# Optimization experiments

Measured on AMD Instinct MI355X. Metric: run time of the kernel, lower is better.

Reference implementation:

```python
import jax, jax.numpy as jnp
import numpy as np

N, E = 50000, 800000
F_IN, HID, H, LBL = 512, 16, 8, 40
HC = HID * H  # 128
BN_EPS = 1e-5
ELU_ALPHA = 0.2
NEG_SLOPE = 0.2


def setup_inputs() -> dict:
    key = jax.random.key(0)
    ks = jax.random.split(key, 32)
    inp = {}
    inp['x'] = jax.random.normal(ks[0], (N, F_IN), dtype=jnp.float32)
    inp['edge_index'] = jax.random.randint(ks[1], (2, E), 0, N, dtype=jnp.int32)
    # layer 0: F_IN -> (H, HID), concat
    inp['W0'] = jax.random.normal(ks[2], (F_IN, HC), dtype=jnp.float32) * 0.05
    inp['as0'] = jax.random.normal(ks[3], (H, HID), dtype=jnp.float32) * 0.1
    inp['ad0'] = jax.random.normal(ks[4], (H, HID), dtype=jnp.float32) * 0.1
    inp['b0'] = jnp.zeros((HC,), jnp.float32)
    inp['g0'] = jnp.ones((HC,), jnp.float32)
    inp['be0'] = jnp.zeros((HC,), jnp.float32)
    inp['rm0'] = jnp.zeros((HC,), jnp.float32)
    inp['rv0'] = jnp.ones((HC,), jnp.float32)
    # layer 1: HC -> (H, HID), concat
    inp['W1'] = jax.random.normal(ks[5], (HC, HC), dtype=jnp.float32) * 0.1
    inp['as1'] = jax.random.normal(ks[6], (H, HID), dtype=jnp.float32) * 0.1
    inp['ad1'] = jax.random.normal(ks[7], (H, HID), dtype=jnp.float32) * 0.1
    inp['b1'] = jnp.zeros((HC,), jnp.float32)
    inp['g1'] = jnp.ones((HC,), jnp.float32)
    inp['be1'] = jnp.zeros((HC,), jnp.float32)
    inp['rm1'] = jnp.zeros((HC,), jnp.float32)
    inp['rv1'] = jnp.ones((HC,), jnp.float32)
    # layer 2: HC -> (1, LBL), mean (concat=False)
    inp['W2'] = jax.random.normal(ks[8], (HC, LBL), dtype=jnp.float32) * 0.1
    inp['as2'] = jax.random.normal(ks[9], (1, LBL), dtype=jnp.float32) * 0.1
    inp['ad2'] = jax.random.normal(ks[10], (1, LBL), dtype=jnp.float32) * 0.1
    inp['b2'] = jnp.zeros((LBL,), jnp.float32)
    return inp


def _gat_conv(xf, src, dst, W, a_src, a_dst, b, heads, out_ch, concat):
    # PyG GATConv (eval): linear -> per-head attn logits -> segment softmax over dst -> scatter-add
    n = xf.shape[0]
    h = (xf @ W).reshape(n, heads, out_ch)            # [N,H,C]
    alpha_s = jnp.einsum('nhc,hc->nh', h, a_src)      # [N,H]
    alpha_d = jnp.einsum('nhc,hc->nh', h, a_dst)
    e = jax.nn.leaky_relu(alpha_s[src] + alpha_d[dst], NEG_SLOPE)  # [Etot,H]
    m = jax.ops.segment_max(e, dst, num_segments=n)
    e = jnp.exp(e - m[dst])
    s = jax.ops.segment_sum(e, dst, num_segments=n)
    alpha = e / (s[dst] + 1e-16)                      # [Etot,H]
    msg = alpha[:, :, None] * h[src]                  # [Etot,H,C]
    out = jax.ops.segment_sum(msg, dst, num_segments=n)  # [N,H,C]
    out = out.reshape(n, heads * out_ch) if concat else out.mean(axis=1)
    return out + b


def _bn_elu(xf, g, be, rm, rv):
    y = (xf - rm) * (g * jax.lax.rsqrt(rv + BN_EPS)) + be
    return jnp.where(y > 0, y, ELU_ALPHA * jnp.expm1(y))


def reference(x, edge_index, W0, as0, ad0, b0, g0, be0, rm0, rv0,
              W1, as1, ad1, b1, g1, be1, rm1, rv1, W2, as2, ad2, b2):
    n = x.shape[0]
    # add self-loops (PyG GATConv default add_self_loops=True)
    loops = jnp.arange(n, dtype=edge_index.dtype)
    src = jnp.concatenate([edge_index[0], loops])
    dst = jnp.concatenate([edge_index[1], loops])
    h = _gat_conv(x, src, dst, W0, as0, ad0, b0, H, HID, True)
    h = _bn_elu(h, g0, be0, rm0, rv0)
    h = _gat_conv(h, src, dst, W1, as1, ad1, b1, H, HID, True)
    h = _bn_elu(h, g1, be1, rm1, rv1)
    out = _gat_conv(h, src, dst, W2, as2, ad2, b2, 1, LBL, False)
    return out
```

## Files before the change

kernel.cpp:

```cpp
#include <hip/hip_runtime.h>
#include <hip/hip_bf16.h>
#include <cstdint>
#include <cstddef>

#define NN 50000
#define EE 800000
#define FIN 512
#define HIDC 16
#define NH 8
#define HCH 128
#define NLBL 40
#define NLBLP 48
#define ETOT (EE + NN)
#define NEG_SLOPE 0.2f
#define ELU_A 0.2f
#define BN_EPS 1e-5f

typedef __attribute__((ext_vector_type(8))) short bf16x8;
typedef __attribute__((ext_vector_type(4))) float f32x4;

__device__ inline short f2b(float f) {
    __hip_bfloat16 h = __float2bfloat16(f);
    return *reinterpret_cast<short*>(&h);
}
__device__ inline float blo(unsigned int u) {
    union { unsigned int u; float f; } v; v.u = u << 16; return v.f;
}
__device__ inline float bhi(unsigned int u) {
    union { unsigned int u; float f; } v; v.u = u & 0xffff0000u; return v.f;
}

__global__ __launch_bounds__(256) void k_convW(const float* __restrict__ W,
                                               short* __restrict__ Wt,
                                               int K, int N, int Np)
{
    int idx = blockIdx.x * blockDim.x + threadIdx.x;
    if (idx >= Np * K) return;
    int n = idx / K, k = idx - n * K;
    float v = (n < N) ? W[(size_t)k * N + n] : 0.f;
    Wt[idx] = f2b(v);
}

template<int KDIM, int NTILES, bool A_BF16>
__global__ __launch_bounds__(256) void k_gemm_lds(const void* __restrict__ Ap,
                                                  const short* __restrict__ Wt,
                                                  short* __restrict__ C,
                                                  int M, int N)
{
    constexpr int NFULL = NTILES * 16;
    constexpr int KCH = 128;
    constexpr int NK = KDIM / 32;
    constexpr int NCH = KDIM / KCH;
    constexpr int LROW = KCH + 8;
    __shared__ short Bs[NFULL * LROW];

    const int tid  = threadIdx.x;
    const int wave = tid >> 6;
    const int lane = tid & 63;
    const int quad = lane >> 4;
    const int col  = lane & 15;
    const int cb   = blockIdx.y * NFULL;
    const int row  = blockIdx.x * 64 + wave * 16 + col;
    const int arow = row < M ? row : M - 1;

    f32x4 acc[NTILES];
    #pragma unroll
    for (int t = 0; t < NTILES; ++t) acc[t] = (f32x4){0.f, 0.f, 0.f, 0.f};

    bf16x8 arB[4];
    float4 arF[4][2];
    const short* Ab = (const short*)Ap;
    const float* Af = (const float*)Ap;
    auto pf = [&](int ks) {
        if (ks >= NK) return;
        if (A_BF16) {
            arB[ks & 3] = *(const bf16x8*)(Ab + (size_t)arow * KDIM + ks * 32 + quad * 8);
        } else {
            const float4* p = (const float4*)(Af + (size_t)arow * KDIM + ks * 32 + quad * 8);
            arF[ks & 3][0] = p[0];
            arF[ks & 3][1] = p[1];
        }
    };
    pf(0); pf(1); pf(2); pf(3);

    for (int c = 0; c < NCH; ++c) {
        const int k0 = c * KCH;
        constexpr int TOT8 = NFULL * (KCH / 8);
        #pragma unroll
        for (int i = tid; i < TOT8; i += 256) {
            int n  = i >> 4;
            int kk = i & 15;
            bf16x8 v = *(const bf16x8*)(Wt + (size_t)(cb + n) * KDIM + k0 + kk * 8);
            *(bf16x8*)(Bs + n * LROW + kk * 8) = v;
        }
        __syncthreads();
        #pragma unroll
        for (int s = 0; s < KCH / 32; ++s) {
            const int ks = c * (KCH / 32) + s;
            bf16x8 afrag;
            if (A_BF16) {
                afrag = arB[ks & 3];
            } else {
                float4 v0 = arF[ks & 3][0], v1 = arF[ks & 3][1];
                afrag[0] = f2b(v0.x); afrag[1] = f2b(v0.y);
                afrag[2] = f2b(v0.z); afrag[3] = f2b(v0.w);
                afrag[4] = f2b(v1.x); afrag[5] = f2b(v1.y);
                afrag[6] = f2b(v1.z); afrag[7] = f2b(v1.w);
            }
            pf(ks + 4);
            #pragma unroll
            for (int t = 0; t < NTILES; ++t) {
                bf16x8 bfrag = *(const bf16x8*)(Bs + (t * 16 + col) * LROW + s * 32 + quad * 8);
                acc[t] = __builtin_amdgcn_mfma_f32_16x16x32_bf16(afrag, bfrag, acc[t], 0, 0, 0);
            }
        }
        if (c + 1 < NCH) __syncthreads();
    }

    const int mbase = blockIdx.x * 64 + wave * 16 + quad * 4;
    #pragma unroll
    for (int t = 0; t < NTILES; ++t) {
        int cc = cb + t * 16 + col;
        if (cc < N) {
            #pragma unroll
            for (int r = 0; r < 4; ++r) {
                int m = mbase + r;
                if (m < M) C[(size_t)m * N + cc] = f2b(acc[t][r]);
            }
        }
    }
}

__global__ __launch_bounds__(256) void k_alpha(const unsigned short* __restrict__ h,
                                               const float* __restrict__ a_s,
                                               const float* __restrict__ a_d,
                                               float* __restrict__ as_o,
                                               float* __restrict__ ad_o)
{
    int idx = blockIdx.x * blockDim.x + threadIdx.x;
    if (idx >= NN * NH) return;
    int hh = idx & (NH - 1);
    const uint4* hp = (const uint4*)(h + (size_t)idx * HIDC);
    uint4 q0 = hp[0], q1 = hp[1];
    unsigned int u[8] = {q0.x, q0.y, q0.z, q0.w, q1.x, q1.y, q1.z, q1.w};
    const float* ap = a_s + hh * HIDC;
    const float* dp = a_d + hh * HIDC;
    float ss = 0.f, dd = 0.f;
    #pragma unroll
    for (int i = 0; i < 8; ++i) {
        float f0 = blo(u[i]), f1 = bhi(u[i]);
        ss += f0 * ap[2 * i] + f1 * ap[2 * i + 1];
        dd += f0 * dp[2 * i] + f1 * dp[2 * i + 1];
    }
    as_o[idx] = ss;
    ad_o[idx] = dd;
}

__global__ __launch_bounds__(256) void k_alpha2(const unsigned short* __restrict__ h2,
                                                const float* __restrict__ a_s,
                                                const float* __restrict__ a_d,
                                                float* __restrict__ as_o,
                                                float* __restrict__ ad_o)
{
    int n = blockIdx.x * blockDim.x + threadIdx.x;
    if (n >= NN) return;
    const uint4* hp = (const uint4*)(h2 + (size_t)n * NLBL);
    float ss = 0.f, dd = 0.f;
    #pragma unroll
    for (int qi = 0; qi < 5; ++qi) {
        uint4 q = hp[qi];
        unsigned int u[4] = {q.x, q.y, q.z, q.w};
        #pragma unroll
        for (int j = 0; j < 4; ++j) {
            int c = qi * 8 + j * 2;
            float f0 = blo(u[j]), f1 = bhi(u[j]);
            ss += f0 * a_s[c] + f1 * a_s[c + 1];
            dd += f0 * a_d[c] + f1 * a_d[c + 1];
        }
    }
    as_o[n] = ss;
    ad_o[n] = dd;
}

__global__ __launch_bounds__(256) void k_hist(const int* __restrict__ ei,
                                              int* __restrict__ deg)
{
    int e = blockIdx.x * blockDim.x + threadIdx.x;
    if (e >= ETOT) return;
    int dst = (e < EE) ? ei[EE + e] : (e - EE);
    atomicAdd(&deg[dst], 1);
}

__global__ __launch_bounds__(1024) void k_scan(const int* __restrict__ deg,
                                               int* __restrict__ row_ptr,
                                               int* __restrict__ cursor)
{
    __shared__ int sm[1024];
    __shared__ int carry;
    int tid = threadIdx.x;
    if (tid == 0) carry = 0;
    __syncthreads();
    for (int base = 0; base < NN; base += 8192) {
        int v[8];
        int s = 0;
        int i0 = base + tid * 8;
        #pragma unroll
        for (int j = 0; j < 8; ++j) {
            int i = i0 + j;
            v[j] = (i < NN) ? deg[i] : 0;
            s += v[j];
        }
        sm[tid] = s;
        __syncthreads();
        for (int ofs = 1; ofs < 1024; ofs <<= 1) {
            int t = (tid >= ofs) ? sm[tid - ofs] : 0;
            __syncthreads();
            sm[tid] += t;
            __syncthreads();
        }
        int excl = sm[tid] - s + carry;
        #pragma unroll
        for (int j = 0; j < 8; ++j) {
            int i = i0 + j;
            if (i < NN) { row_ptr[i] = excl; cursor[i] = excl; }
            excl += v[j];
        }
        int total = sm[1023];
        __syncthreads();
        if (tid == 0) carry += total;
        __syncthreads();
    }
    if (tid == 0) row_ptr[NN] = carry;
}

__global__ __launch_bounds__(256) void k_scatter(const int* __restrict__ ei,
                                                 int* __restrict__ cursor,
                                                 int* __restrict__ csr_src)
{
    int e = blockIdx.x * blockDim.x + threadIdx.x;
    if (e >= ETOT) return;
    int src, dst;
    if (e < EE) { src = ei[e]; dst = ei[EE + e]; }
    else        { src = dst = e - EE; }
    int pos = atomicAdd(&cursor[dst], 1);
    csr_src[pos] = src;
}

__global__ __launch_bounds__(256) void k_agg(const int* __restrict__ row_ptr,
                                             const int* __restrict__ csr_src,
                                             const unsigned short* __restrict__ h,
                                             const float* __restrict__ as,
                                             const float* __restrict__ ad,
                                             const float* __restrict__ b,
                                             const float* __restrict__ g,
                                             const float* __restrict__ be,
                                             const float* __restrict__ rm,
                                             const float* __restrict__ rv,
                                             short* __restrict__ out)
{
    int n = blockIdx.x * 4 + (threadIdx.x >> 6);
    if (n >= NN) return;
    int lane = threadIdx.x & 63;
    int half = lane >> 5;
    int c4 = lane & 31;
    int hh = c4 >> 2;
    float adv = ad[n * NH + hh];
    float a0 = 0.f, a1 = 0.f, a2 = 0.f, a3 = 0.f, sw = 0.f;
    int jb = row_ptr[n], je = row_ptr[n + 1];
    int j = jb + half;
    for (; j + 6 < je; j += 8) {
        int s0 = csr_src[j];
        int s1 = csr_src[j + 2];
        int s2 = csr_src[j + 4];
        int s3 = csr_src[j + 6];
        float l0 = as[s0 * NH + hh] + adv;
        float l1 = as[s1 * NH + hh] + adv;
        float l2 = as[s2 * NH + hh] + adv;
        float l3 = as[s3 * NH + hh] + adv;
        uint2 u0 = *(const uint2*)(h + (size_t)s0 * HCH + 4 * c4);
        uint2 u1 = *(const uint2*)(h + (size_t)s1 * HCH + 4 * c4);
        uint2 u2 = *(const uint2*)(h + (size_t)s2 * HCH + 4 * c4);
        uint2 u3 = *(const uint2*)(h + (size_t)s3 * HCH + 4 * c4);
        l0 = l0 > 0.f ? l0 : NEG_SLOPE * l0;
        l1 = l1 > 0.f ? l1 : NEG_SLOPE * l1;
        l2 = l2 > 0.f ? l2 : NEG_SLOPE * l2;
        l3 = l3 > 0.f ? l3 : NEG_SLOPE * l3;
        float w0 = __expf(l0), w1 = __expf(l1), w2 = __expf(l2), w3 = __expf(l3);
        sw += (w0 + w1) + (w2 + w3);
        a0 += w0 * blo(u0.x) + w1 * blo(u1.x) + w2 * blo(u2.x) + w3 * blo(u3.x);
        a1 += w0 * bhi(u0.x) + w1 * bhi(u1.x) + w2 * bhi(u2.x) + w3 * bhi(u3.x);
        a2 += w0 * blo(u0.y) + w1 * blo(u1.y) + w2 * blo(u2.y) + w3 * blo(u3.y);
        a3 += w0 * bhi(u0.y) + w1 * bhi(u1.y) + w2 * bhi(u2.y) + w3 * bhi(u3.y);
    }
    for (; j < je; j += 2) {
        int s0 = csr_src[j];
        float l0 = as[s0 * NH + hh] + adv;
        uint2 u0 = *(const uint2*)(h + (size_t)s0 * HCH + 4 * c4);
        l0 = l0 > 0.f ? l0 : NEG_SLOPE * l0;
        float w0 = __expf(l0);
        sw += w0;
        a0 += w0 * blo(u0.x);
        a1 += w0 * bhi(u0.x);
        a2 += w0 * blo(u0.y);
        a3 += w0 * bhi(u0.y);
    }
    a0 += __shfl_down(a0, 32);
    a1 += __shfl_down(a1, 32);
    a2 += __shfl_down(a2, 32);
    a3 += __shfl_down(a3, 32);
    sw += __shfl_down(sw, 32);
    if (half == 0) {
        int c = 4 * c4;
        float inv = 1.f / (sw + 1e-16f);
        float4 bv  = *(const float4*)(b + c);
        float4 gv  = *(const float4*)(g + c);
        float4 bev = *(const float4*)(be + c);
        float4 rmv = *(const float4*)(rm + c);
        float4 rvv = *(const float4*)(rv + c);
        float r0 = a0 * inv + bv.x;
        float r1 = a1 * inv + bv.y;
        float r2 = a2 * inv + bv.z;
        float r3 = a3 * inv + bv.w;
        r0 = (r0 - rmv.x) * (gv.x * rsqrtf(rvv.x + BN_EPS)) + bev.x;
        r1 = (r1 - rmv.y) * (gv.y * rsqrtf(rvv.y + BN_EPS)) + bev.y;
        r2 = (r2 - rmv.z) * (gv.z * rsqrtf(rvv.z + BN_EPS)) + bev.z;
        r3 = (r3 - rmv.w) * (gv.w * rsqrtf(rvv.w + BN_EPS)) + bev.w;
        r0 = r0 > 0.f ? r0 : ELU_A * expm1f(r0);
        r1 = r1 > 0.f ? r1 : ELU_A * expm1f(r1);
        r2 = r2 > 0.f ? r2 : ELU_A * expm1f(r2);
        r3 = r3 > 0.f ? r3 : ELU_A * expm1f(r3);
        unsigned int lo = (unsigned int)(unsigned short)f2b(r0) |
                          ((unsigned int)(unsigned short)f2b(r1) << 16);
        unsigned int hi = (unsigned int)(unsigned short)f2b(r2) |
                          ((unsigned int)(unsigned short)f2b(r3) << 16);
        *(uint2*)(out + (size_t)n * HCH + c) = make_uint2(lo, hi);
    }
}

__global__ __launch_bounds__(256) void k_agg2(const int* __restrict__ row_ptr,
                                              const int* __restrict__ csr_src,
                                              const unsigned short* __restrict__ h2,
                                              const float* __restrict__ as,
                                              const float* __restrict__ ad,
                                              const float* __restrict__ b,
                                              float* __restrict__ out)
{
    int n = blockIdx.x * 4 + (threadIdx.x >> 6);
    if (n >= NN) return;
    int lane = threadIdx.x & 63;
    int half = lane >> 5;
    int c2 = lane & 31;
    bool act = c2 < 20;
    int coff = act ? 2 * c2 : 0;
    float adv = ad[n];
    float acc0 = 0.f, acc1 = 0.f, sw = 0.f;
    int jb = row_ptr[n], je = row_ptr[n + 1];
    int j = jb + half;
    for (; j + 6 < je; j += 8) {
        int s0 = csr_src[j];
        int s1 = csr_src[j + 2];
        int s2 = csr_src[j + 4];
        int s3 = csr_src[j + 6];
        float l0 = as[s0] + adv;
        float l1 = as[s1] + adv;
        float l2 = as[s2] + adv;
        float l3 = as[s3] + adv;
        unsigned int u0 = *(const unsigned int*)(h2 + (size_t)s0 * NLBL + coff);
        unsigned int u1 = *(const unsigned int*)(h2 + (size_t)s1 * NLBL + coff);
        unsigned int u2 = *(const unsigned int*)(h2 + (size_t)s2 * NLBL + coff);
        unsigned int u3 = *(const unsigned int*)(h2 + (size_t)s3 * NLBL + coff);
        l0 = l0 > 0.f ? l0 : NEG_SLOPE * l0;
        l1 = l1 > 0.f ? l1 : NEG_SLOPE * l1;
        l2 = l2 > 0.f ? l2 : NEG_SLOPE * l2;
        l3 = l3 > 0.f ? l3 : NEG_SLOPE * l3;
        float w0 = __expf(l0), w1 = __expf(l1), w2 = __expf(l2), w3 = __expf(l3);
        sw += (w0 + w1) + (w2 + w3);
        if (act) {
            acc0 += w0 * blo(u0) + w1 * blo(u1) + w2 * blo(u2) + w3 * blo(u3);
            acc1 += w0 * bhi(u0) + w1 * bhi(u1) + w2 * bhi(u2) + w3 * bhi(u3);
        }
    }
    for (; j < je; j += 2) {
        int s = csr_src[j];
        float l = as[s] + adv;
        unsigned int u = *(const unsigned int*)(h2 + (size_t)s * NLBL + coff);
        l = l > 0.f ? l : NEG_SLOPE * l;
        float w = __expf(l);
        sw += w;
        if (act) {
            acc0 += w * blo(u);
            acc1 += w * bhi(u);
        }
    }
    float acc0b = __shfl_down(acc0, 32);
    float acc1b = __shfl_down(acc1, 32);
    float swb   = __shfl_down(sw, 32);
    if (half == 0 && act) {
        acc0 += acc0b; acc1 += acc1b; sw += swb;
        float inv = 1.f / (sw + 1e-16f);
        out[(size_t)n * NLBL + 2 * c2]     = acc0 * inv + b[2 * c2];
        out[(size_t)n * NLBL + 2 * c2 + 1] = acc1 * inv + b[2 * c2 + 1];
    }
}

extern "C" void kernel_launch(void* const* d_in, const int* in_sizes, int n_in,
                              void* d_out, int out_size, void* d_ws, size_t ws_size,
                              hipStream_t stream)
{
    const float* x   = (const float*)d_in[0];
    const int*   ei  = (const int*)d_in[1];
    const float* W0  = (const float*)d_in[2];
    const float* as0 = (const float*)d_in[3];
    const float* ad0 = (const float*)d_in[4];
    const float* b0  = (const float*)d_in[5];
    const float* g0  = (const float*)d_in[6];
    const float* be0 = (const float*)d_in[7];
    const float* rm0 = (const float*)d_in[8];
    const float* rv0 = (const float*)d_in[9];
    const float* W1  = (const float*)d_in[10];
    const float* as1 = (const float*)d_in[11];
    const float* ad1 = (const float*)d_in[12];
    const float* b1  = (const float*)d_in[13];
    const float* g1  = (const float*)d_in[14];
    const float* be1 = (const float*)d_in[15];
    const float* rm1 = (const float*)d_in[16];
    const float* rv1 = (const float*)d_in[17];
    const float* W2  = (const float*)d_in[18];
    const float* a_s2 = (const float*)d_in[19];
    const float* a_d2 = (const float*)d_in[20];
    const float* b2  = (const float*)d_in[21];
    float* out = (float*)d_out;

    char* ws = (char*)d_ws;
    size_t off = 0;
    auto alloc = [&](size_t bytes) {
        void* p = (void*)(ws + off);
        off += (bytes + 255) & ~(size_t)255;
        return p;
    };
    short* hbuf   = (short*)alloc((size_t)NN * HCH * 2);
    short* fbuf   = (short*)alloc((size_t)NN * HCH * 2);
    float* asb    = (float*)alloc((size_t)NN * NH * 4);
    float* adb    = (float*)alloc((size_t)NN * NH * 4);
    int*   deg    = (int*)alloc((size_t)NN * 4);
    int*   rowp   = (int*)alloc((size_t)(NN + 1) * 4);
    int*   cursor = (int*)alloc((size_t)NN * 4);
    int*   csrs   = (int*)alloc((size_t)ETOT * 4);
    short* Wt0    = (short*)alloc((size_t)HCH * FIN * 2);
    short* Wt1    = (short*)alloc((size_t)HCH * HCH * 2);
    short* Wt2    = (short*)alloc((size_t)NLBLP * HCH * 2);
    short* h2     = hbuf;

    const int T = 256;
    const int gE  = (ETOT + T - 1) / T;
    const int gNH = (NN * NH + T - 1) / T;
    const int gN4 = (NN + 3) / 4;
    const int gM  = (NN + 63) / 64;

    k_convW<<<(HCH * FIN + T - 1) / T, T, 0, stream>>>(W0, Wt0, FIN, HCH, HCH);
    k_convW<<<(HCH * HCH + T - 1) / T, T, 0, stream>>>(W1, Wt1, HCH, HCH, HCH);
    k_convW<<<(NLBLP * HCH + T - 1) / T, T, 0, stream>>>(W2, Wt2, HCH, NLBL, NLBLP);

    hipMemsetAsync(deg, 0, (size_t)NN * 4, stream);
    k_hist<<<gE, T, 0, stream>>>(ei, deg);
    k_scan<<<1, 1024, 0, stream>>>(deg, rowp, cursor);
    k_scatter<<<gE, T, 0, stream>>>(ei, cursor, csrs);

    k_gemm_lds<FIN, 4, false><<<dim3(gM, 2), T, 0, stream>>>(x, Wt0, hbuf, NN, HCH);
    k_alpha<<<gNH, T, 0, stream>>>((const unsigned short*)hbuf, as0, ad0, asb, adb);
    k_agg<<<gN4, T, 0, stream>>>(rowp, csrs, (const unsigned short*)hbuf, asb, adb,
                                 b0, g0, be0, rm0, rv0, fbuf);

    k_gemm_lds<HCH, 4, true><<<dim3(gM, 2), T, 0, stream>>>(fbuf, Wt1, hbuf, NN, HCH);
    k_alpha<<<gNH, T, 0, stream>>>((const unsigned short*)hbuf, as1, ad1, asb, adb);
    k_agg<<<gN4, T, 0, stream>>>(rowp, csrs, (const unsigned short*)hbuf, asb, adb,
                                 b1, g1, be1, rm1, rv1, fbuf);

    k_gemm_lds<HCH, 3, true><<<dim3(gM, 1), T, 0, stream>>>(fbuf, Wt2, h2, NN, NLBL);
    k_alpha2<<<(NN + T - 1) / T, T, 0, stream>>>((const unsigned short*)h2, a_s2, a_d2, asb, adb);
    k_agg2<<<gN4, T, 0, stream>>>(rowp, csrs, (const unsigned short*)h2, asb, adb, b2, out);
}
```

Measured before the change: 482.2 us.

## Add LDS-staged GEMM covering full 128-wide output per block with register prefetch

Adds a new GEMM kernel in which each 512-thread block computes a 64x128 output tile. Both A and B are staged through LDS, and the next K chunk is prefetched into registers while MFMA runs on the current one. Previously the grid was split in two along N, so the fp32 x matrix was read twice; now it is read once per row block. The new kernel is used for layers 0 and 1. The cost is more LDS per block, which may reduce occupancy.

```diff
diff --git a/kernel.cpp b/kernel.cpp
--- a/kernel.cpp
+++ b/kernel.cpp
@@ -17,6 +17,7 @@
 #define BN_EPS 1e-5f
 
 typedef __attribute__((ext_vector_type(8))) short bf16x8;
+typedef __attribute__((ext_vector_type(4))) short bf16x4;
 typedef __attribute__((ext_vector_type(4))) float f32x4;
 
 __device__ inline short f2b(float f) {
@@ -39,6 +40,116 @@
     int n = idx / K, k = idx - n * K;
     float v = (n < N) ? W[(size_t)k * N + n] : 0.f;
     Wt[idx] = f2b(v);
+}
+
+template<int KDIM, bool A_BF16>
+__global__ __launch_bounds__(512, 4) void k_gemm2(const void* __restrict__ Ap,
+                                                  const short* __restrict__ Wt,
+                                                  short* __restrict__ C,
+                                                  int M)
+{
+    constexpr int KCH  = 128;
+    constexpr int NCH  = KDIM / KCH;
+    constexpr int LROW = KCH + 8;
+    __shared__ short As[64 * LROW];
+    __shared__ short Bs[128 * LROW];
+
+    const int tid  = threadIdx.x;
+    const int wv   = tid >> 6;
+    const int lane = tid & 63;
+    const int quad = lane >> 4;
+    const int col  = lane & 15;
+    const int wr   = wv >> 1;
+    const int wn   = wv & 1;
+    const int rowbase = blockIdx.x * 64;
+
+    const float* Af = (const float*)Ap;
+    const short* Ab = (const short*)Ap;
+
+    float4 pa[4];
+    bf16x8 pab[2];
+    bf16x8 pb[4];
+
+    auto loadA = [&](int c) {
+        if constexpr (A_BF16) {
+            #pragma unroll
+            for (int r = 0; r < 2; ++r) {
+                int gr = rowbase + r * 32 + (tid >> 4);
+                gr = gr < M ? gr : M - 1;
+                pab[r] = *(const bf16x8*)(Ab + (size_t)gr * KDIM + c * KCH + (tid & 15) * 8);
+            }
+        } else {
+            #pragma unroll
+            for (int r = 0; r < 4; ++r) {
+                int gr = rowbase + r * 16 + (tid >> 5);
+                gr = gr < M ? gr : M - 1;
+                pa[r] = *(const float4*)(Af + (size_t)gr * KDIM + c * KCH + (tid & 31) * 4);
+            }
+        }
+    };
+    auto loadB = [&](int c) {
+        #pragma unroll
+        for (int r = 0; r < 4; ++r) {
+            int n = r * 32 + (tid >> 4);
+            pb[r] = *(const bf16x8*)(Wt + (size_t)n * KDIM + c * KCH + (tid & 15) * 8);
+        }
+    };
+    auto writeAB = [&]() {
+        if constexpr (A_BF16) {
+            #pragma unroll
+            for (int r = 0; r < 2; ++r) {
+                int row = r * 32 + (tid >> 4);
+                *(bf16x8*)(As + row * LROW + (tid & 15) * 8) = pab[r];
+            }
+        } else {
+            #pragma unroll
+            for (int r = 0; r < 4; ++r) {
+                int row = r * 16 + (tid >> 5);
+                bf16x4 w;
+                w[0] = f2b(pa[r].x); w[1] = f2b(pa[r].y);
+                w[2] = f2b(pa[r].z); w[3] = f2b(pa[r].w);
+                *(bf16x4*)(As + row * LROW + (tid & 31) * 4) = w;
+            }
+        }
+        #pragma unroll
+        for (int r = 0; r < 4; ++r) {
+            int n = r * 32 + (tid >> 4);
+            *(bf16x8*)(Bs + n * LROW + (tid & 15) * 8) = pb[r];
+        }
+    };
+
+    f32x4 acc[4];
+    #pragma unroll
+    for (int t = 0; t < 4; ++t) acc[t] = (f32x4){0.f, 0.f, 0.f, 0.f};
+
+    loadA(0); loadB(0);
+
+    for (int c = 0; c < NCH; ++c) {
+        writeAB();
+        __syncthreads();
+        if (c + 1 < NCH) { loadA(c + 1); loadB(c + 1); }
+        #pragma unroll
+        for (int s = 0; s < KCH / 32; ++s) {
+            bf16x8 af = *(const bf16x8*)(As + (wr * 16 + col) * LROW + s * 32 + quad * 8);
+            #pragma unroll
+            for (int t = 0; t < 4; ++t) {
+                bf16x8 bf = *(const bf16x8*)(Bs + (wn * 64 + t * 16 + col) * LROW + s * 32 + quad * 8);
+                acc[t] = __builtin_amdgcn_mfma_f32_16x16x32_bf16(af, bf, acc[t], 0, 0, 0);
+            }
+        }
+        if (c + 1 < NCH) __syncthreads();
+    }
+
+    const int mb = rowbase + wr * 16 + quad * 4;
+    #pragma unroll
+    for (int t = 0; t < 4; ++t) {
+        int cc = wn * 64 + t * 16 + col;
+        #pragma unroll
+        for (int r = 0; r < 4; ++r) {
+            int m = mb + r;
+            if (m < M) C[(size_t)m * HCH + cc] = f2b(acc[t][r]);
+        }
+    }
 }
 
 template<int KDIM, int NTILES, bool A_BF16>
@@ -466,12 +577,12 @@
     k_scan<<<1, 1024, 0, stream>>>(deg, rowp, cursor);
     k_scatter<<<gE, T, 0, stream>>>(ei, cursor, csrs);
 
-    k_gemm_lds<FIN, 4, false><<<dim3(gM, 2), T, 0, stream>>>(x, Wt0, hbuf, NN, HCH);
+    k_gemm2<FIN, false><<<gM, 512, 0, stream>>>(x, Wt0, hbuf, NN);
     k_alpha<<<gNH, T, 0, stream>>>((const unsigned short*)hbuf, as0, ad0, asb, adb);
     k_agg<<<gN4, T, 0, stream>>>(rowp, csrs, (const unsigned short*)hbuf, asb, adb,
                                  b0, g0, be0, rm0, rv0, fbuf);
 
-    k_gemm_lds<HCH, 4, true><<<dim3(gM, 2), T, 0, stream>>>(fbuf, Wt1, hbuf, NN, HCH);
+    k_gemm2<HCH, true><<<gM, 512, 0, stream>>>(fbuf, Wt1, hbuf, NN);
     k_alpha<<<gNH, T, 0, stream>>>((const unsigned short*)hbuf, as1, ad1, asb, adb);
     k_agg<<<gN4, T, 0, stream>>>(rowp, csrs, (const unsigned short*)hbuf, asb, adb,
                                  b1, g1, be1, rm1, rv1, fbuf);
```

New measurement: 465.1 us. 3.5% less time.
